# Kernel optimization log

Measured on AMD Instinct MI355X. Metric: run time of the kernel, lower is better.

Reference implementation:

```python
import jax, jax.numpy as jnp
import numpy as np

TAU = 0.95
MARGIN = 1.0
NUM_NEG = 1

B, S = 4096, 4096
N_RERANK = 8192


def setup_inputs() -> dict:
    key = jax.random.key(0)
    k1, k2, k3 = jax.random.split(key, 3)
    rerank_y = jax.random.normal(k1, (N_RERANK, 1), dtype=jnp.float32)
    # probabilities in (0,1]; keep away from 0 since the loss takes log
    cut_y = jax.random.uniform(k2, (B, S, 1), dtype=jnp.float32, minval=1e-4, maxval=1.0)
    rerank_label = jnp.ones((B, 1), dtype=jnp.float32)  # unused (overwritten by ones in source)
    cut_label = jax.random.randint(k3, (B, S), 0, 2, dtype=jnp.int32)
    return {"rerank_y": rerank_y, "cut_y": cut_y, "rerank_label": rerank_label, "cut_label": cut_label}


def _f1_weights(cut_label):
    # Vectorized Metric_for_Loss.f1(labels[i], j): F1 at cut depth j+1.
    lab = cut_label.astype(jnp.float32)                      # [B,S]
    cum = jnp.cumsum(lab, axis=1)                            # relevant docs within top j+1
    k = jnp.arange(1, lab.shape[1] + 1, dtype=jnp.float32)   # cut depth
    total = jnp.sum(lab, axis=1, keepdims=True)              # total relevant per list
    prec = cum / k
    rec = jnp.where(total > 0, cum / jnp.maximum(total, 1.0), 0.0)
    den = prec + rec
    return jnp.where(den > 0, 2.0 * prec * rec / den, 0.0)   # [B,S]


def _attncut_loss(cut_y, cut_label):
    out2d = jnp.squeeze(cut_y, axis=2)                       # [B,S]
    r = _f1_weights(cut_label)
    # Faithful to source: q = exp(r/tau) is summed into norm_factor, then q := 1/norm_factor
    norm = jnp.sum(jnp.exp(r / TAU), axis=1, keepdims=True)  # [B,1]
    q = 1.0 / norm
    loss_mat = jnp.log(out2d) * q
    return -jnp.sum(loss_mat) / out2d.shape[0]


def _rerank_loss(rerank_y):
    y_pos = rerank_y[:: NUM_NEG + 1, :]                      # [B,1]
    y_neg = rerank_y[1 :: NUM_NEG + 1, :]                    # [B,1] (num_neg=1 -> cat of one)
    y_neg = jnp.mean(y_neg, axis=-1, keepdims=True)
    # margin_ranking_loss with y=1, reduction='mean'
    return jnp.mean(jnp.maximum(0.0, -(y_pos - y_neg) + MARGIN))


def reference(rerank_y, cut_y, rerank_label, cut_label):
    return _attncut_loss(cut_y, cut_label) + _rerank_loss(rerank_y)
```

## Files before the change

### kernel.cpp

```cpp
#include <hip/hip_runtime.h>

#define NROWS 4096
#define NCOLS 4096
#define TAU 0.95f
#define MARGIN 1.0f
#define INV_TAU (1.0f / TAU)
#define LN2F 0.69314718056f

__global__ __launch_bounds__(256, 4) void attncut_kernel(
    const float* __restrict__ cut_y, const int* __restrict__ cut_label,
    float* __restrict__ partials) {
  const int t = threadIdx.x;
  const int lane = t & 63;
  const int wid = t >> 6;
  const int row = (blockIdx.x << 2) | wid;

  const size_t rbase = (size_t)row * NCOLS;
  const int4* lb = (const int4*)(cut_label + rbase) + lane * 16;
  const float4* yb = (const float4*)(cut_y + rbase) + lane * 16;

  unsigned int blo = 0u, bhi = 0u;
#pragma unroll
  for (int j = 0; j < 8; ++j) {
    const int4 L = lb[j];
    const unsigned int nib =
        (unsigned int)(L.x | (L.y << 1) | (L.z << 2) | (L.w << 3));
    blo |= nib << (4 * j);
  }
#pragma unroll
  for (int j = 0; j < 8; ++j) {
    const int4 L = lb[j + 8];
    const unsigned int nib =
        (unsigned int)(L.x | (L.y << 1) | (L.z << 2) | (L.w << 3));
    bhi |= nib << (4 * j);
  }
  const int lsum = __popc(blo) + __popc(bhi);

  float l2 = 0.f;
#pragma unroll
  for (int j = 0; j < 16; ++j) {
    const float4 v = yb[j];
    l2 += __log2f((v.x * v.y) * (v.z * v.w));
  }

  int x = lsum;
#pragma unroll
  for (int off = 1; off < 64; off <<= 1) {
    const int v = __shfl_up(x, off, 64);
    if (lane >= off) x += v;
  }
  const int Ttot = __shfl(x, 63, 64);
  const float Tf = (float)Ttot;
  float cf = (float)(x - lsum);

  const float kb = (float)(lane * 64) + Tf;
  float na = 0.f;
#pragma unroll
  for (int j = 0; j < 32; ++j) {
    cf += (float)((blo >> j) & 1u);
    const float r =
        (cf > 0.f) ? __fdividef(2.0f * cf, kb + (float)(j + 1)) : 0.f;
    na += __expf(r * INV_TAU);
  }
#pragma unroll
  for (int j = 0; j < 32; ++j) {
    cf += (float)((bhi >> j) & 1u);
    const float r =
        (cf > 0.f) ? __fdividef(2.0f * cf, kb + (float)(j + 33)) : 0.f;
    na += __expf(r * INV_TAU);
  }

#pragma unroll
  for (int off = 32; off > 0; off >>= 1) {
    na += __shfl_down(na, off, 64);
    l2 += __shfl_down(l2, off, 64);
  }
  if (lane == 0) {
    partials[row] = -(l2 * LN2F) / (na * (float)NROWS);
  }
}

__global__ __launch_bounds__(256) void finish_kernel(
    const float* __restrict__ partials, const float* __restrict__ rerank_y,
    float* __restrict__ out) {
  const int t = threadIdx.x;
  const int lane = t & 63, wid = t >> 6;

  float acc = 0.f;
  const float4* p4 = (const float4*)partials;
#pragma unroll
  for (int i = 0; i < 4; ++i) {
    float4 v = p4[t + 256 * i];
    acc += (v.x + v.y) + (v.z + v.w);
  }

  float racc = 0.f;
  const float4* y4 = (const float4*)rerank_y;
#pragma unroll
  for (int i = 0; i < 8; ++i) {
    float4 v = y4[t + 256 * i];
    racc += fmaxf(0.f, MARGIN - (v.x - v.y));
    racc += fmaxf(0.f, MARGIN - (v.z - v.w));
  }
  acc += racc * (1.0f / 4096.0f);

#pragma unroll
  for (int off = 32; off > 0; off >>= 1) acc += __shfl_down(acc, off, 64);
  __shared__ float ws[4];
  if (lane == 0) ws[wid] = acc;
  __syncthreads();
  if (t == 0) out[0] = (ws[0] + ws[1]) + (ws[2] + ws[3]);
}

extern "C" void kernel_launch(void* const* d_in, const int* in_sizes, int n_in,
                              void* d_out, int out_size, void* d_ws, size_t ws_size,
                              hipStream_t stream) {
  const float* rerank_y = (const float*)d_in[0];
  const float* cut_y = (const float*)d_in[1];
  const int* cut_label = (const int*)d_in[3];
  float* out = (float*)d_out;
  float* partials = (float*)d_ws;

  attncut_kernel<<<NROWS / 4, 256, 0, stream>>>(cut_y, cut_label, partials);
  finish_kernel<<<1, 256, 0, stream>>>(partials, rerank_y, out);
}
```

Measured before the change: 164.9 us.

## Split attncut into coalesced log and F1-norm kernels with ballot-based prefix sums

The fused per-row kernel is split into two kernels: one that sums log(cut_y) and one that computes the F1 softmax normaliser from labels. Both now use interleaved, coalesced float4/int4 loads (lane + 64*j) instead of giving each lane a contiguous 256-byte chunk. The label prefix count uses wave ballots and mbcnt per nibble position in place of a shuffle scan. This adds an extra kernel launch and a read-modify-write of the partials buffer between kernels.

```diff
diff --git a/kernel.cpp b/kernel.cpp
--- a/kernel.cpp
+++ b/kernel.cpp
@@ -7,76 +7,91 @@
 #define INV_TAU (1.0f / TAU)
 #define LN2F 0.69314718056f
 
-__global__ __launch_bounds__(256, 4) void attncut_kernel(
-    const float* __restrict__ cut_y, const int* __restrict__ cut_label,
-    float* __restrict__ partials) {
+
+__device__ __forceinline__ int mbcnt64(unsigned long long m) {
+  return __builtin_amdgcn_mbcnt_hi(
+      (unsigned int)(m >> 32),
+      __builtin_amdgcn_mbcnt_lo((unsigned int)m, 0));
+}
+
+__global__ __launch_bounds__(256, 4) void ylog_kernel(
+    const float* __restrict__ cut_y, float* __restrict__ partials) {
   const int t = threadIdx.x;
   const int lane = t & 63;
   const int wid = t >> 6;
   const int row = (blockIdx.x << 2) | wid;
+  const float4* yb = (const float4*)(cut_y + (size_t)row * NCOLS);
 
-  const size_t rbase = (size_t)row * NCOLS;
-  const int4* lb = (const int4*)(cut_label + rbase) + lane * 16;
-  const float4* yb = (const float4*)(cut_y + rbase) + lane * 16;
+  float l2 = 0.f;
+#pragma unroll
+  for (int j = 0; j < 16; ++j) {
+    const float4 v = yb[lane + 64 * j];
+    l2 += __log2f((v.x * v.y) * (v.z * v.w));
+  }
+#pragma unroll
+  for (int off = 32; off > 0; off >>= 1) l2 += __shfl_down(l2, off, 64);
+  if (lane == 0) partials[row] = l2 * LN2F;
+}
+
+__global__ __launch_bounds__(256, 4) void norm_kernel(
+    const int* __restrict__ cut_label, float* __restrict__ partials) {
+  const int t = threadIdx.x;
+  const int lane = t & 63;
+  const int wid = t >> 6;
+  const int row = (blockIdx.x << 2) | wid;
+  const int4* lb = (const int4*)(cut_label + (size_t)row * NCOLS);
 
   unsigned int blo = 0u, bhi = 0u;
 #pragma unroll
   for (int j = 0; j < 8; ++j) {
-    const int4 L = lb[j];
-    const unsigned int nib =
-        (unsigned int)(L.x | (L.y << 1) | (L.z << 2) | (L.w << 3));
-    blo |= nib << (4 * j);
+    const int4 L = lb[lane + 64 * j];
+    blo |= (unsigned int)(L.x | (L.y << 1) | (L.z << 2) | (L.w << 3))
+           << (4 * j);
   }
 #pragma unroll
   for (int j = 0; j < 8; ++j) {
-    const int4 L = lb[j + 8];
-    const unsigned int nib =
-        (unsigned int)(L.x | (L.y << 1) | (L.z << 2) | (L.w << 3));
-    bhi |= nib << (4 * j);
+    const int4 L = lb[lane + 64 * (j + 8)];
+    bhi |= (unsigned int)(L.x | (L.y << 1) | (L.z << 2) | (L.w << 3))
+           << (4 * j);
   }
-  const int lsum = __popc(blo) + __popc(bhi);
 
-  float l2 = 0.f;
+  int ls = __popc(blo) + __popc(bhi);
+#pragma unroll
+  for (int off = 32; off > 0; off >>= 1) ls += __shfl_down(ls, off, 64);
+  const float Tf = (float)__shfl(ls, 0, 64);
+
+  float na = 0.f;
+  float Cf = 0.f;
 #pragma unroll
   for (int j = 0; j < 16; ++j) {
-    const float4 v = yb[j];
-    l2 += __log2f((v.x * v.y) * (v.z * v.w));
-  }
+    const unsigned int nib =
+        ((j < 8) ? (blo >> (4 * j)) : (bhi >> (4 * (j - 8)))) & 0xFu;
+    const unsigned long long b0 = __ballot(nib & 1u);
+    const unsigned long long b1 = __ballot(nib & 2u);
+    const unsigned long long b2 = __ballot(nib & 4u);
+    const unsigned long long b3 = __ballot(nib & 8u);
+    const int before = mbcnt64(b0) + mbcnt64(b1) + mbcnt64(b2) + mbcnt64(b3);
 
-  int x = lsum;
-#pragma unroll
-  for (int off = 1; off < 64; off <<= 1) {
-    const int v = __shfl_up(x, off, 64);
-    if (lane >= off) x += v;
-  }
-  const int Ttot = __shfl(x, 63, 64);
-  const float Tf = (float)Ttot;
-  float cf = (float)(x - lsum);
+    float c = Cf + (float)before;
+    const float kb = (float)(4 * (64 * j + lane)) + Tf;
 
-  const float kb = (float)(lane * 64) + Tf;
-  float na = 0.f;
-#pragma unroll
-  for (int j = 0; j < 32; ++j) {
-    cf += (float)((blo >> j) & 1u);
-    const float r =
-        (cf > 0.f) ? __fdividef(2.0f * cf, kb + (float)(j + 1)) : 0.f;
-    na += __expf(r * INV_TAU);
-  }
-#pragma unroll
-  for (int j = 0; j < 32; ++j) {
-    cf += (float)((bhi >> j) & 1u);
-    const float r =
-        (cf > 0.f) ? __fdividef(2.0f * cf, kb + (float)(j + 33)) : 0.f;
-    na += __expf(r * INV_TAU);
+    c += (float)(nib & 1u);
+    na += __expf(((c > 0.f) ? __fdividef(2.0f * c, kb + 1.0f) : 0.f) * INV_TAU);
+    c += (float)((nib >> 1) & 1u);
+    na += __expf(((c > 0.f) ? __fdividef(2.0f * c, kb + 2.0f) : 0.f) * INV_TAU);
+    c += (float)((nib >> 2) & 1u);
+    na += __expf(((c > 0.f) ? __fdividef(2.0f * c, kb + 3.0f) : 0.f) * INV_TAU);
+    c += (float)((nib >> 3) & 1u);
+    na += __expf(((c > 0.f) ? __fdividef(2.0f * c, kb + 4.0f) : 0.f) * INV_TAU);
+
+    Cf += (float)(__popcll(b0) + __popcll(b1) + __popcll(b2) + __popcll(b3));
   }
 
 #pragma unroll
-  for (int off = 32; off > 0; off >>= 1) {
-    na += __shfl_down(na, off, 64);
-    l2 += __shfl_down(l2, off, 64);
-  }
+  for (int off = 32; off > 0; off >>= 1) na += __shfl_down(na, off, 64);
   if (lane == 0) {
-    partials[row] = -(l2 * LN2F) / (na * (float)NROWS);
+    const float lnsum = partials[row];
+    partials[row] = -lnsum / (na * (float)NROWS);
   }
 }
 
@@ -121,6 +136,7 @@
   float* out = (float*)d_out;
   float* partials = (float*)d_ws;
 
-  attncut_kernel<<<NROWS / 4, 256, 0, stream>>>(cut_y, cut_label, partials);
+  ylog_kernel<<<NROWS / 4, 256, 0, stream>>>(cut_y, partials);
+  norm_kernel<<<NROWS / 4, 256, 0, stream>>>(cut_label, partials);
   finish_kernel<<<1, 256, 0, stream>>>(partials, rerank_y, out);
 }
```

Result: faster. 158.6 us (-3.8%).
